# Kernel optimization log

Hardware: AMD Instinct MI355X
Metric: run time of the kernel (lower is better)

The kernel has to match this reference:

```python
import jax, jax.numpy as jnp
import numpy as np

DIM = 512
NUM_HEADS = 8
HEAD_DIM = DIM // NUM_HEADS
B, S = 2, 2048


def setup_inputs() -> dict:
    key = jax.random.key(0)
    ks = jax.random.split(key, 16)
    scale = 1.0 / np.sqrt(DIM)
    inp = {
        "x": jax.random.normal(ks[0], (B, S, DIM), dtype=jnp.float32),
        "Qexpl": jax.random.normal(ks[1], (B, S, DIM), dtype=jnp.float32),
        "Kexpl": jax.random.normal(ks[2], (B, S, DIM), dtype=jnp.float32),
        "fl": jax.random.uniform(ks[3], (B,), dtype=jnp.float32),
        "fu": jax.random.uniform(ks[4], (B,), dtype=jnp.float32),
        "age": jax.random.uniform(ks[5], (B,), dtype=jnp.float32),
        "gender": jax.random.uniform(ks[6], (B,), dtype=jnp.float32),
        # Linear params: weight stored as [out, in] like torch; y = x @ W.T + b
        "Wq": jax.random.normal(ks[7], (DIM, DIM), dtype=jnp.float32) * scale,
        "bq": jnp.zeros((DIM,), dtype=jnp.float32),
        "Wk": jax.random.normal(ks[8], (DIM, DIM), dtype=jnp.float32) * scale,
        "bk": jnp.zeros((DIM,), dtype=jnp.float32),
        "Wv": jax.random.normal(ks[9], (DIM, DIM), dtype=jnp.float32) * scale,
        "bv": jnp.zeros((DIM,), dtype=jnp.float32),
        "Wo": jax.random.normal(ks[10], (DIM, DIM), dtype=jnp.float32) * scale,
        "bo": jnp.zeros((DIM,), dtype=jnp.float32),
    }
    return inp


def reference(x, Qexpl, Kexpl, fl, fu, age, gender, Wq, bq, Wk, bk, Wv, bv, Wo, bo):
    # drofe_fn is None -> Q/K projections used directly.
    Q = Qexpl @ Wq.T + bq            # [B, S, D]
    K = Kexpl @ Wk.T + bk            # [B, S, D]
    V = x @ Wv.T + bv                # [B, S, D]

    def split_heads(t):  # [B, S, D] -> [B, H, S, hd]
        return t.reshape(B, S, NUM_HEADS, HEAD_DIM).transpose(0, 2, 1, 3)

    Qh, Kh, Vh = split_heads(Q), split_heads(K), split_heads(V)
    scale = 1.0 / np.sqrt(HEAD_DIM).astype(np.float32)
    scores = jnp.einsum("bhqd,bhkd->bhqk", Qh, Kh) * scale  # [B, H, S, S]
    weights = jax.nn.softmax(scores, axis=-1)
    attn = jnp.einsum("bhqk,bhkd->bhqd", weights, Vh)        # [B, H, S, hd]
    attn = attn.transpose(0, 2, 1, 3).reshape(B, S, DIM)
    return attn @ Wo.T + bo
```

## Files before the change

kernel.cpp:

```cpp
#include <hip/hip_runtime.h>
#include <hip/hip_bf16.h>

typedef unsigned short ushort_t;
typedef __attribute__((ext_vector_type(8))) short bf16x8;
typedef __attribute__((ext_vector_type(4))) float f32x4;

__device__ __forceinline__ ushort_t f2bf(float f) {
    union { float f; unsigned u; } v; v.f = f;
    unsigned r = v.u + 0x7FFF + ((v.u >> 16) & 1);
    return (ushort_t)(r >> 16);
}
__device__ __forceinline__ bf16x8 ld8(const ushort_t* p) { return *(const bf16x8*)p; }

__device__ __forceinline__ unsigned cvt2(float x, float y) {
    __hip_bfloat162 h = __float22bfloat162_rn(make_float2(x, y));
    unsigned r; __builtin_memcpy(&r, &h, 4); return r;
}
__device__ __forceinline__ bf16x8 pack8f(float4 a, float4 b) {
    union { unsigned u[4]; bf16x8 v; } o;
    o.u[0] = cvt2(a.x, a.y); o.u[1] = cvt2(a.z, a.w);
    o.u[2] = cvt2(b.x, b.y); o.u[3] = cvt2(b.z, b.w);
    return o.v;
}

__device__ __forceinline__ void gload_lds16(const ushort_t* g, ushort_t* l) {
    __builtin_amdgcn_global_load_lds(
        (const __attribute__((address_space(1))) void*)g,
        (__attribute__((address_space(3))) void*)l, 16, 0, 0);
}

__global__ __launch_bounds__(256, 2)
void proj_qkv_kernel(const float* __restrict__ Qe, const float* __restrict__ Ke,
                     const float* __restrict__ x,
                     const float* __restrict__ Wq, const float* __restrict__ Wk,
                     const float* __restrict__ Wv,
                     const float* __restrict__ bq, const float* __restrict__ bk,
                     const float* __restrict__ bv,
                     ushort_t* __restrict__ Qo, ushort_t* __restrict__ Ko,
                     ushort_t* __restrict__ Vt)
{
    __shared__ ushort_t smem[2 * 128 * 72];
    ushort_t* lA = smem;
    ushort_t* lB = smem + 128 * 72;

    const int z = blockIdx.z;
    const float* A = (z == 0) ? Qe : (z == 1) ? Ke : x;
    const float* W = (z == 0) ? Wq : (z == 1) ? Wk : Wv;
    const float* bias = (z == 0) ? bq : (z == 1) ? bk : bv;

    const int m0 = blockIdx.y * 128, n0 = blockIdx.x * 128;
    const int t = threadIdx.x;
    const int lane = t & 63, wave = t >> 6;
    const int wm = (wave & 1) * 64, wn = (wave >> 1) * 64;
    const int fr = lane & 15, quad = lane >> 4;

    f32x4 acc[4][4] = {};
    float4 fa[4][2], fw[4][2];

#pragma unroll
    for (int i = 0; i < 4; ++i) {
        int s = i * 256 + t;
        int r = s >> 3, jp = s & 7;
        const float* pa = A + (size_t)(m0 + r) * 512 + jp * 8;
        fa[i][0] = *(const float4*)pa; fa[i][1] = *(const float4*)(pa + 4);
        const float* pw = W + (size_t)(n0 + r) * 512 + jp * 8;
        fw[i][0] = *(const float4*)pw; fw[i][1] = *(const float4*)(pw + 4);
    }

    for (int kk = 0; kk < 8; ++kk) {
        if (kk) __syncthreads();
#pragma unroll
        for (int i = 0; i < 4; ++i) {
            int s = i * 256 + t;
            int r = s >> 3, jp = s & 7;
            *(bf16x8*)(lA + r * 72 + jp * 8) = pack8f(fa[i][0], fa[i][1]);
            *(bf16x8*)(lB + r * 72 + jp * 8) = pack8f(fw[i][0], fw[i][1]);
        }
        __syncthreads();
        if (kk < 7) {
            int k0 = (kk + 1) * 64;
#pragma unroll
            for (int i = 0; i < 4; ++i) {
                int s = i * 256 + t;
                int r = s >> 3, jp = s & 7;
                const float* pa = A + (size_t)(m0 + r) * 512 + k0 + jp * 8;
                fa[i][0] = *(const float4*)pa; fa[i][1] = *(const float4*)(pa + 4);
                const float* pw = W + (size_t)(n0 + r) * 512 + k0 + jp * 8;
                fw[i][0] = *(const float4*)pw; fw[i][1] = *(const float4*)(pw + 4);
            }
        }

#pragma unroll
        for (int ks = 0; ks < 2; ++ks) {
            bf16x8 af[4], bfrag[4];
#pragma unroll
            for (int mt = 0; mt < 4; ++mt)
                af[mt] = ld8(lA + (wm + mt * 16 + fr) * 72 + (ks * 4 + quad) * 8);
#pragma unroll
            for (int nt = 0; nt < 4; ++nt)
                bfrag[nt] = ld8(lB + (wn + nt * 16 + fr) * 72 + (ks * 4 + quad) * 8);
#pragma unroll
            for (int mt = 0; mt < 4; ++mt)
#pragma unroll
                for (int nt = 0; nt < 4; ++nt)
                    acc[mt][nt] = __builtin_amdgcn_mfma_f32_16x16x32_bf16(
                        af[mt], bfrag[nt], acc[mt][nt], 0, 0, 0);
        }
    }

    const float C1 = 0.125f * 1.44269504088896340736f;
    if (z != 2) {
        ushort_t* dst = (z == 0) ? Qo : Ko;
#pragma unroll
        for (int nt = 0; nt < 4; ++nt) {
            int n = n0 + wn + nt * 16 + fr;
            float bb = bias[n];
#pragma unroll
            for (int mt = 0; mt < 4; ++mt) {
                int mb = m0 + wm + mt * 16 + quad * 4;
                if (z == 0) {
#pragma unroll
                    for (int r = 0; r < 4; ++r)
                        dst[(size_t)(mb + r) * 512 + n] = f2bf((acc[mt][nt][r] + bb) * C1);
                } else {
#pragma unroll
                    for (int r = 0; r < 4; ++r)
                        dst[(size_t)(mb + r) * 512 + n] = f2bf(acc[mt][nt][r] + bb);
                }
            }
        }
    } else {
        __syncthreads();
        ushort_t* lT = smem;
#pragma unroll
        for (int nt = 0; nt < 4; ++nt) {
            int nl = wn + nt * 16 + fr;
            float bb = bias[n0 + nl];
#pragma unroll
            for (int mt = 0; mt < 4; ++mt) {
                int tm = wm + mt * 16 + quad * 4;
#pragma unroll
                for (int r = 0; r < 4; ++r) {
                    int tl = tm + r;
                    int sg = 8 * (tl & 15) + ((tl >> 4) & 7);
                    lT[nl * 136 + sg] = f2bf(acc[mt][nt][r] + bb);
                }
            }
        }
        __syncthreads();
        const int bidx = m0 >> 11, m0t = m0 & 2047;
#pragma unroll
        for (int i = 0; i < 8; ++i) {
            int s = i * 256 + t;
            int row = s >> 4, c = s & 15;
            int n = n0 + row;
            int h = n >> 6, d = n & 63;
            bf16x8 v = ld8(lT + row * 136 + c * 8);
            *(bf16x8*)(Vt + ((size_t)((bidx * 8 + h) * 64 + d)) * 2048 + m0t + c * 8) = v;
        }
    }
}

__global__ __launch_bounds__(256, 2)
void gemm_o_kernel(const ushort_t* __restrict__ A, const float* __restrict__ W,
                   const float* __restrict__ bias, float* __restrict__ dst)
{
    __shared__ ushort_t lA[64 * 72];
    __shared__ ushort_t lB[64 * 72];
    const int m0 = blockIdx.y * 64, n0 = blockIdx.x * 64;
    const int t = threadIdx.x;
    const int lane = t & 63, wave = t >> 6;
    const int wm = (wave & 1) * 32, wn = (wave >> 1) * 32;
    const int fr = lane & 15, quad = lane >> 4;

    f32x4 acc[2][2] = {};
    bf16x8 va[2];
    float4 fw[2][2];

#pragma unroll
    for (int i = 0; i < 2; ++i) {
        int s = i * 256 + t;
        int r = s >> 3, jp = s & 7;
        va[i] = ld8(A + (size_t)(m0 + r) * 512 + jp * 8);
        const float* p = W + (size_t)(n0 + r) * 512 + jp * 8;
        fw[i][0] = *(const float4*)p; fw[i][1] = *(const float4*)(p + 4);
    }

    for (int kk = 0; kk < 8; ++kk) {
        if (kk) __syncthreads();
#pragma unroll
        for (int i = 0; i < 2; ++i) {
            int s = i * 256 + t;
            int r = s >> 3, jp = s & 7;
            *(bf16x8*)(lA + r * 72 + jp * 8) = va[i];
            *(bf16x8*)(lB + r * 72 + jp * 8) = pack8f(fw[i][0], fw[i][1]);
        }
        __syncthreads();
        if (kk < 7) {
            int k0 = (kk + 1) * 64;
#pragma unroll
            for (int i = 0; i < 2; ++i) {
                int s = i * 256 + t;
                int r = s >> 3, jp = s & 7;
                va[i] = ld8(A + (size_t)(m0 + r) * 512 + k0 + jp * 8);
                const float* p = W + (size_t)(n0 + r) * 512 + k0 + jp * 8;
                fw[i][0] = *(const float4*)p; fw[i][1] = *(const float4*)(p + 4);
            }
        }

        bf16x8 af[2][2], bfrag[2][2];
#pragma unroll
        for (int ks = 0; ks < 2; ++ks) {
#pragma unroll
            for (int mt = 0; mt < 2; ++mt)
                af[mt][ks] = ld8(lA + (wm + mt * 16 + fr) * 72 + (ks * 4 + quad) * 8);
#pragma unroll
            for (int nt = 0; nt < 2; ++nt)
                bfrag[nt][ks] = ld8(lB + (wn + nt * 16 + fr) * 72 + (ks * 4 + quad) * 8);
        }
#pragma unroll
        for (int ks = 0; ks < 2; ++ks)
#pragma unroll
            for (int mt = 0; mt < 2; ++mt)
#pragma unroll
                for (int nt = 0; nt < 2; ++nt)
                    acc[mt][nt] = __builtin_amdgcn_mfma_f32_16x16x32_bf16(
                        af[mt][ks], bfrag[nt][ks], acc[mt][nt], 0, 0, 0);
    }

#pragma unroll
    for (int nt = 0; nt < 2; ++nt) {
        int n = n0 + wn + nt * 16 + fr;
        float bb = bias[n];
#pragma unroll
        for (int mt = 0; mt < 2; ++mt) {
            int mb = m0 + wm + mt * 16 + quad * 4;
#pragma unroll
            for (int r = 0; r < 4; ++r)
                dst[(size_t)(mb + r) * 512 + n] = acc[mt][nt][r] + bb;
        }
    }
}

__global__ __launch_bounds__(256, 3)
void attn_kernel(const ushort_t* __restrict__ Q, const ushort_t* __restrict__ K,
                 const ushort_t* __restrict__ Vt, float* __restrict__ Opart,
                 float* __restrict__ Lsum)
{
    __shared__ ushort_t lK[128 * 64];
    __shared__ ushort_t lV[64 * 128];
    __shared__ ushort_t lP[64 * 128];

    const int b = blockIdx.z >> 1, half = blockIdx.z & 1;
    const int h = blockIdx.y;
    const int q0 = blockIdx.x * 64;
    const int kvbase = half * 1024;
    const int t = threadIdx.x;
    const int lane = t & 63, w = t >> 6;
    const int wq = w * 16;
    const int fr = lane & 15, quad = lane >> 4;
    const int fr7 = fr & 7;

    bf16x8 aq[2];
    {
        const ushort_t* qp = Q + (size_t)(b * 2048 + q0 + wq + fr) * 512 + h * 64 + quad * 8;
        aq[0] = ld8(qp);
        aq[1] = ld8(qp + 32);
    }

    const int krl = w * 32 + (lane >> 3);
    const ushort_t* kg = K + (size_t)(b * 2048 + kvbase + krl) * 512 + h * 64
                           + (lane & 7) * 8;
    ushort_t* lk_wr = lK + krl * 64 + (((lane & 7) ^ (krl & 7)) << 3);

    const int vrl = w * 4 + (lane >> 4);
    const ushort_t* vbase = Vt + (size_t)((b * 8 + h) * 64 + vrl) * 2048 + kvbase
                              + (((lane & 15) ^ (vrl & 7)) << 3);

    const ushort_t* kr0 = lK + fr * 64 + ((quad ^ fr7) << 3);
    const ushort_t* kr1 = lK + fr * 64 + (((4 + quad) ^ fr7) << 3);
    const ushort_t* vr[4];
    const ushort_t* pr[4];
#pragma unroll
    for (int ks = 0; ks < 4; ++ks) {
        int cs = (((ks * 4 + quad) ^ fr7) << 3);
        vr[ks] = lV + fr * 128 + cs;
        pr[ks] = lP + (wq + fr) * 128 + cs;
    }
    ushort_t* pw[4];
#pragma unroll
    for (int r = 0; r < 4; ++r) {
        int row = wq + quad * 4 + r;
        pw[r] = lP + row * 128 + ((fr ^ (row & 7)) << 3);
    }

    bf16x8 kreg[4];
#pragma unroll
    for (int i = 0; i < 4; ++i)
        kreg[i] = ld8(kg + (size_t)(i * 8) * 512);
#pragma unroll
    for (int i = 0; i < 4; ++i)
        *(bf16x8*)(lk_wr + i * 8 * 64) = kreg[i];
    __syncthreads();

    f32x4 oacc[4] = {};
    float lpart[4] = {};

    for (int tt = 0; tt < 8; ++tt) {
        const int kv = tt << 7;

#pragma unroll
        for (int i = 0; i < 4; ++i)
            gload_lds16(vbase + kv + (size_t)(i * 16) * 2048, lV + (i * 16 + w * 4) * 128);
        __builtin_amdgcn_sched_barrier(0);
        if (tt < 7) {
#pragma unroll
            for (int i = 0; i < 4; ++i)
                kreg[i] = ld8(kg + (size_t)(kv + 128 + i * 8) * 512);
        }
        __builtin_amdgcn_sched_barrier(0);

        f32x4 sc[8] = {};
#pragma unroll
        for (int nt = 0; nt < 8; ++nt) {
            bf16x8 kb = ld8(kr0 + nt * 16 * 64);
            sc[nt] = __builtin_amdgcn_mfma_f32_16x16x32_bf16(aq[0], kb, sc[nt], 0, 0, 0);
        }
#pragma unroll
        for (int nt = 0; nt < 8; ++nt) {
            bf16x8 kb = ld8(kr1 + nt * 16 * 64);
            sc[nt] = __builtin_amdgcn_mfma_f32_16x16x32_bf16(aq[1], kb, sc[nt], 0, 0, 0);
        }

#pragma unroll
        for (int r = 0; r < 4; ++r) {
            float pv[8]; float acc = 0.f;
#pragma unroll
            for (int nt = 0; nt < 8; ++nt) { pv[nt] = exp2f(sc[nt][r]); acc += pv[nt]; }
            lpart[r] += acc;
            union { unsigned u[4]; bf16x8 v; } pu;
            pu.u[0] = cvt2(pv[0], pv[1]); pu.u[1] = cvt2(pv[2], pv[3]);
            pu.u[2] = cvt2(pv[4], pv[5]); pu.u[3] = cvt2(pv[6], pv[7]);
            *(bf16x8*)pw[r] = pu.v;
        }

        if (tt < 7) asm volatile("s_waitcnt vmcnt(4)" ::: "memory");
        else        asm volatile("s_waitcnt vmcnt(0)" ::: "memory");
        __builtin_amdgcn_s_barrier();
        __builtin_amdgcn_sched_barrier(0);

        if (tt < 7) {
#pragma unroll
            for (int i = 0; i < 4; ++i)
                *(bf16x8*)(lk_wr + i * 8 * 64) = kreg[i];
        }

#pragma unroll
        for (int ks = 0; ks < 4; ++ks) {
            bf16x8 ap = ld8(pr[ks]);
#pragma unroll
            for (int nt = 0; nt < 4; ++nt) {
                bf16x8 vb = ld8(vr[ks] + nt * 16 * 128);
                oacc[nt] = __builtin_amdgcn_mfma_f32_16x16x32_bf16(ap, vb, oacc[nt], 0, 0, 0);
            }
        }
        __syncthreads();
    }

#pragma unroll
    for (int r = 0; r < 4; ++r) {
        float rs = lpart[r];
#pragma unroll
        for (int o = 1; o < 16; o <<= 1)
            rs += __shfl_xor(rs, o, 64);
        int qrow = q0 + wq + quad * 4 + r;
        float* od = Opart + ((size_t)(half * 2 + b) * 2048 + qrow) * 512 + h * 64;
#pragma unroll
        for (int nt = 0; nt < 4; ++nt)
            od[nt * 16 + fr] = oacc[nt][r];
        if (fr == 0)
            Lsum[((half * 2 + b) * 8 + h) * 2048 + qrow] = rs;
    }
}

__global__ __launch_bounds__(256)
void merge_kernel(const float* __restrict__ Opart, const float* __restrict__ Lsum,
                  ushort_t* __restrict__ Ows)
{
    int gid = blockIdx.x * 256 + threadIdx.x;
    int row = gid >> 7;
    int c4 = (gid & 127) << 2;
    int b = row >> 11, q = row & 2047;
    int h = c4 >> 6;
    float l0 = Lsum[(b * 8 + h) * 2048 + q];
    float l1 = Lsum[((2 + b) * 8 + h) * 2048 + q];
    float inv = 1.f / (l0 + l1);
    float4 o0 = *(const float4*)(Opart + (size_t)row * 512 + c4);
    float4 o1 = *(const float4*)(Opart + (size_t)(row + 4096) * 512 + c4);
    union { unsigned u[2]; } o;
    o.u[0] = cvt2((o0.x + o1.x) * inv, (o0.y + o1.y) * inv);
    o.u[1] = cvt2((o0.z + o1.z) * inv, (o0.w + o1.w) * inv);
    unsigned* dst = (unsigned*)(Ows + (size_t)row * 512 + c4);
    dst[0] = o.u[0];
    dst[1] = o.u[1];
}

extern "C" void kernel_launch(void* const* d_in, const int* in_sizes, int n_in,
                              void* d_out, int out_size, void* d_ws, size_t ws_size,
                              hipStream_t stream) {
    const float* x   = (const float*)d_in[0];
    const float* Qe  = (const float*)d_in[1];
    const float* Ke  = (const float*)d_in[2];
    const float* Wq  = (const float*)d_in[7];
    const float* bq  = (const float*)d_in[8];
    const float* Wk  = (const float*)d_in[9];
    const float* bk  = (const float*)d_in[10];
    const float* Wv  = (const float*)d_in[11];
    const float* bv  = (const float*)d_in[12];
    const float* Wo  = (const float*)d_in[13];
    const float* bo  = (const float*)d_in[14];

    const size_t NTOK = 2 * 2048;
    const size_t ACT = NTOK * 512;

    ushort_t* p = (ushort_t*)d_ws;
    ushort_t* Qws = p; p += ACT;
    ushort_t* Kws = p; p += ACT;
    ushort_t* Vt  = p; p += ACT;
    ushort_t* Ows = p; p += ACT;
    float* Opart = (float*)p;
    float* Lsum  = Opart + 2 * ACT;

    proj_qkv_kernel<<<dim3(4, 32, 3), 256, 0, stream>>>(Qe, Ke, x, Wq, Wk, Wv,
                                                        bq, bk, bv, Qws, Kws, Vt);
    attn_kernel<<<dim3(32, 8, 4), 256, 0, stream>>>(Qws, Kws, Vt, Opart, Lsum);
    merge_kernel<<<dim3(2048), 256, 0, stream>>>(Opart, Lsum, Ows);
    gemm_o_kernel<<<dim3(8, 64), 256, 0, stream>>>(Ows, Wo, bo, (float*)d_out);
}
```

Measured before the change: 168.4 us.

## Keep softmax probabilities in registers and fuse merge into output projection

The attention kernel now computes S^T by swapping the MFMA operands, so each lane's score accumulators line up with the A-operand layout of the PV MFMA. The exponentiated probabilities are packed to bf16 in registers instead of going through an LDS P tile, and the V staging permutation in the QKV projection is changed to match. The LDS saving allows raising occupancy to 4 blocks per CU, and setprio is added around the MFMA sections. The separate merge kernel is removed: the output GEMM now reads both fp32 partial outputs and row sums directly, normalizing and converting to bf16 while staging. That reads twice as many fp32 bytes per GEMM tile in exchange for dropping one launch and a round trip through memory.

```diff
diff --git a/kernel.cpp b/kernel.cpp
--- a/kernel.cpp
+++ b/kernel.cpp
@@ -142,7 +142,7 @@
 #pragma unroll
                 for (int r = 0; r < 4; ++r) {
                     int tl = tm + r;
-                    int sg = 8 * (tl & 15) + ((tl >> 4) & 7);
+                    int sg = (tl & 96) + ((tl & 12) << 1) + ((tl >> 4 & 1) << 2) + (tl & 3);
                     lT[nl * 136 + sg] = f2bf(acc[mt][nt][r] + bb);
                 }
             }
@@ -162,8 +162,9 @@
 }
 
 __global__ __launch_bounds__(256, 2)
-void gemm_o_kernel(const ushort_t* __restrict__ A, const float* __restrict__ W,
-                   const float* __restrict__ bias, float* __restrict__ dst)
+void gemm_o_kernel(const float* __restrict__ Opart, const float* __restrict__ Lsum,
+                   const float* __restrict__ W, const float* __restrict__ bias,
+                   float* __restrict__ dst)
 {
     __shared__ ushort_t lA[64 * 72];
     __shared__ ushort_t lB[64 * 72];
@@ -172,16 +173,23 @@
     const int lane = t & 63, wave = t >> 6;
     const int wm = (wave & 1) * 32, wn = (wave >> 1) * 32;
     const int fr = lane & 15, quad = lane >> 4;
+    const int bq_ = m0 >> 11;
+    const int qq0 = m0 & 2047;
 
     f32x4 acc[2][2] = {};
-    bf16x8 va[2];
-    float4 fw[2][2];
+    float4 fo0[2][2], fo1[2][2], fw[2][2];
+    float l0[2], l1[2];
 
 #pragma unroll
     for (int i = 0; i < 2; ++i) {
         int s = i * 256 + t;
         int r = s >> 3, jp = s & 7;
-        va[i] = ld8(A + (size_t)(m0 + r) * 512 + jp * 8);
+        const float* p0 = Opart + (size_t)(m0 + r) * 512 + jp * 8;
+        fo0[i][0] = *(const float4*)p0;        fo0[i][1] = *(const float4*)(p0 + 4);
+        fo1[i][0] = *(const float4*)(p0 + 4096 * 512);
+        fo1[i][1] = *(const float4*)(p0 + 4096 * 512 + 4);
+        l0[i] = Lsum[(bq_ * 8 + 0) * 2048 + qq0 + r];
+        l1[i] = Lsum[((2 + bq_) * 8 + 0) * 2048 + qq0 + r];
         const float* p = W + (size_t)(n0 + r) * 512 + jp * 8;
         fw[i][0] = *(const float4*)p; fw[i][1] = *(const float4*)(p + 4);
     }
@@ -192,7 +200,16 @@
         for (int i = 0; i < 2; ++i) {
             int s = i * 256 + t;
             int r = s >> 3, jp = s & 7;
-            *(bf16x8*)(lA + r * 72 + jp * 8) = va[i];
+            float inv = 1.f / (l0[i] + l1[i]);
+            float4 a0 = make_float4((fo0[i][0].x + fo1[i][0].x) * inv,
+                                    (fo0[i][0].y + fo1[i][0].y) * inv,
+                                    (fo0[i][0].z + fo1[i][0].z) * inv,
+                                    (fo0[i][0].w + fo1[i][0].w) * inv);
+            float4 a1 = make_float4((fo0[i][1].x + fo1[i][1].x) * inv,
+                                    (fo0[i][1].y + fo1[i][1].y) * inv,
+                                    (fo0[i][1].z + fo1[i][1].z) * inv,
+                                    (fo0[i][1].w + fo1[i][1].w) * inv);
+            *(bf16x8*)(lA + r * 72 + jp * 8) = pack8f(a0, a1);
             *(bf16x8*)(lB + r * 72 + jp * 8) = pack8f(fw[i][0], fw[i][1]);
         }
         __syncthreads();
@@ -202,7 +219,12 @@
             for (int i = 0; i < 2; ++i) {
                 int s = i * 256 + t;
                 int r = s >> 3, jp = s & 7;
-                va[i] = ld8(A + (size_t)(m0 + r) * 512 + k0 + jp * 8);
+                const float* p0 = Opart + (size_t)(m0 + r) * 512 + k0 + jp * 8;
+                fo0[i][0] = *(const float4*)p0;        fo0[i][1] = *(const float4*)(p0 + 4);
+                fo1[i][0] = *(const float4*)(p0 + 4096 * 512);
+                fo1[i][1] = *(const float4*)(p0 + 4096 * 512 + 4);
+                l0[i] = Lsum[(bq_ * 8 + kk + 1) * 2048 + qq0 + r];
+                l1[i] = Lsum[((2 + bq_) * 8 + kk + 1) * 2048 + qq0 + r];
                 const float* p = W + (size_t)(n0 + r) * 512 + k0 + jp * 8;
                 fw[i][0] = *(const float4*)p; fw[i][1] = *(const float4*)(p + 4);
             }
@@ -242,14 +264,13 @@
     }
 }
 
-__global__ __launch_bounds__(256, 3)
+__global__ __launch_bounds__(256, 4)
 void attn_kernel(const ushort_t* __restrict__ Q, const ushort_t* __restrict__ K,
                  const ushort_t* __restrict__ Vt, float* __restrict__ Opart,
                  float* __restrict__ Lsum)
 {
     __shared__ ushort_t lK[128 * 64];
     __shared__ ushort_t lV[64 * 128];
-    __shared__ ushort_t lP[64 * 128];
 
     const int b = blockIdx.z >> 1, half = blockIdx.z & 1;
     const int h = blockIdx.y;
@@ -279,20 +300,11 @@
 
     const ushort_t* kr0 = lK + fr * 64 + ((quad ^ fr7) << 3);
     const ushort_t* kr1 = lK + fr * 64 + (((4 + quad) ^ fr7) << 3);
-    const ushort_t* vr[4];
-    const ushort_t* pr[4];
-#pragma unroll
-    for (int ks = 0; ks < 4; ++ks) {
-        int cs = (((ks * 4 + quad) ^ fr7) << 3);
-        vr[ks] = lV + fr * 128 + cs;
-        pr[ks] = lP + (wq + fr) * 128 + cs;
-    }
-    ushort_t* pw[4];
-#pragma unroll
-    for (int r = 0; r < 4; ++r) {
-        int row = wq + quad * 4 + r;
-        pw[r] = lP + row * 128 + ((fr ^ (row & 7)) << 3);
-    }
+    const ushort_t* vr0 = lV + fr * 128 + (((0 * 4 + quad) ^ fr7) << 3);
+    const ushort_t* vr1 = lV + fr * 128 + (((1 * 4 + quad) ^ fr7) << 3);
+    const ushort_t* vr2 = lV + fr * 128 + (((2 * 4 + quad) ^ fr7) << 3);
+    const ushort_t* vr3 = lV + fr * 128 + (((3 * 4 + quad) ^ fr7) << 3);
+    const ushort_t* vr[4] = { vr0, vr1, vr2, vr3 };
 
     bf16x8 kreg[4];
 #pragma unroll
@@ -304,7 +316,7 @@
     __syncthreads();
 
     f32x4 oacc[4] = {};
-    float lpart[4] = {};
+    float lsum = 0.f;
 
     for (int tt = 0; tt < 8; ++tt) {
         const int kv = tt << 7;
@@ -321,88 +333,65 @@
         __builtin_amdgcn_sched_barrier(0);
 
         f32x4 sc[8] = {};
+        __builtin_amdgcn_s_setprio(1);
 #pragma unroll
         for (int nt = 0; nt < 8; ++nt) {
             bf16x8 kb = ld8(kr0 + nt * 16 * 64);
-            sc[nt] = __builtin_amdgcn_mfma_f32_16x16x32_bf16(aq[0], kb, sc[nt], 0, 0, 0);
+            sc[nt] = __builtin_amdgcn_mfma_f32_16x16x32_bf16(kb, aq[0], sc[nt], 0, 0, 0);
         }
 #pragma unroll
         for (int nt = 0; nt < 8; ++nt) {
             bf16x8 kb = ld8(kr1 + nt * 16 * 64);
-            sc[nt] = __builtin_amdgcn_mfma_f32_16x16x32_bf16(aq[1], kb, sc[nt], 0, 0, 0);
-        }
-
-#pragma unroll
-        for (int r = 0; r < 4; ++r) {
-            float pv[8]; float acc = 0.f;
-#pragma unroll
-            for (int nt = 0; nt < 8; ++nt) { pv[nt] = exp2f(sc[nt][r]); acc += pv[nt]; }
-            lpart[r] += acc;
-            union { unsigned u[4]; bf16x8 v; } pu;
-            pu.u[0] = cvt2(pv[0], pv[1]); pu.u[1] = cvt2(pv[2], pv[3]);
-            pu.u[2] = cvt2(pv[4], pv[5]); pu.u[3] = cvt2(pv[6], pv[7]);
-            *(bf16x8*)pw[r] = pu.v;
-        }
+            sc[nt] = __builtin_amdgcn_mfma_f32_16x16x32_bf16(kb, aq[1], sc[nt], 0, 0, 0);
+        }
+        __builtin_amdgcn_s_setprio(0);
 
         if (tt < 7) asm volatile("s_waitcnt vmcnt(4)" ::: "memory");
         else        asm volatile("s_waitcnt vmcnt(0)" ::: "memory");
         __builtin_amdgcn_s_barrier();
         __builtin_amdgcn_sched_barrier(0);
 
-        if (tt < 7) {
-#pragma unroll
-            for (int i = 0; i < 4; ++i)
-                *(bf16x8*)(lk_wr + i * 8 * 64) = kreg[i];
-        }
-
+        __builtin_amdgcn_s_setprio(1);
 #pragma unroll
         for (int ks = 0; ks < 4; ++ks) {
-            bf16x8 ap = ld8(pr[ks]);
+            float p0[4], p1[4];
+#pragma unroll
+            for (int r = 0; r < 4; ++r) p0[r] = exp2f(sc[2 * ks][r]);
+#pragma unroll
+            for (int r = 0; r < 4; ++r) p1[r] = exp2f(sc[2 * ks + 1][r]);
+            lsum += ((p0[0] + p0[1]) + (p0[2] + p0[3]))
+                  + ((p1[0] + p1[1]) + (p1[2] + p1[3]));
+            union { unsigned u[4]; bf16x8 v; } pa;
+            pa.u[0] = cvt2(p0[0], p0[1]); pa.u[1] = cvt2(p0[2], p0[3]);
+            pa.u[2] = cvt2(p1[0], p1[1]); pa.u[3] = cvt2(p1[2], p1[3]);
 #pragma unroll
             for (int nt = 0; nt < 4; ++nt) {
                 bf16x8 vb = ld8(vr[ks] + nt * 16 * 128);
-                oacc[nt] = __builtin_amdgcn_mfma_f32_16x16x32_bf16(ap, vb, oacc[nt], 0, 0, 0);
-            }
-        }
+                oacc[nt] = __builtin_amdgcn_mfma_f32_16x16x32_bf16(pa.v, vb, oacc[nt], 0, 0, 0);
+            }
+            if (ks == 0 && tt < 7) {
+#pragma unroll
+                for (int i = 0; i < 4; ++i)
+                    *(bf16x8*)(lk_wr + i * 8 * 64) = kreg[i];
+            }
+        }
+        __builtin_amdgcn_s_setprio(0);
         __syncthreads();
     }
 
+    float rs = lsum;
+    rs += __shfl_xor(rs, 16, 64);
+    rs += __shfl_xor(rs, 32, 64);
 #pragma unroll
     for (int r = 0; r < 4; ++r) {
-        float rs = lpart[r];
-#pragma unroll
-        for (int o = 1; o < 16; o <<= 1)
-            rs += __shfl_xor(rs, o, 64);
         int qrow = q0 + wq + quad * 4 + r;
         float* od = Opart + ((size_t)(half * 2 + b) * 2048 + qrow) * 512 + h * 64;
 #pragma unroll
         for (int nt = 0; nt < 4; ++nt)
             od[nt * 16 + fr] = oacc[nt][r];
-        if (fr == 0)
-            Lsum[((half * 2 + b) * 8 + h) * 2048 + qrow] = rs;
-    }
-}
-
-__global__ __launch_bounds__(256)
-void merge_kernel(const float* __restrict__ Opart, const float* __restrict__ Lsum,
-                  ushort_t* __restrict__ Ows)
-{
-    int gid = blockIdx.x * 256 + threadIdx.x;
-    int row = gid >> 7;
-    int c4 = (gid & 127) << 2;
-    int b = row >> 11, q = row & 2047;
-    int h = c4 >> 6;
-    float l0 = Lsum[(b * 8 + h) * 2048 + q];
-    float l1 = Lsum[((2 + b) * 8 + h) * 2048 + q];
-    float inv = 1.f / (l0 + l1);
-    float4 o0 = *(const float4*)(Opart + (size_t)row * 512 + c4);
-    float4 o1 = *(const float4*)(Opart + (size_t)(row + 4096) * 512 + c4);
-    union { unsigned u[2]; } o;
-    o.u[0] = cvt2((o0.x + o1.x) * inv, (o0.y + o1.y) * inv);
-    o.u[1] = cvt2((o0.z + o1.z) * inv, (o0.w + o1.w) * inv);
-    unsigned* dst = (unsigned*)(Ows + (size_t)row * 512 + c4);
-    dst[0] = o.u[0];
-    dst[1] = o.u[1];
+    }
+    if (lane < 16)
+        Lsum[((half * 2 + b) * 8 + h) * 2048 + q0 + wq + lane] = rs;
 }
 
 extern "C" void kernel_launch(void* const* d_in, const int* in_sizes, int n_in,
@@ -427,13 +416,11 @@
     ushort_t* Qws = p; p += ACT;
     ushort_t* Kws = p; p += ACT;
     ushort_t* Vt  = p; p += ACT;
-    ushort_t* Ows = p; p += ACT;
     float* Opart = (float*)p;
     float* Lsum  = Opart + 2 * ACT;
 
     proj_qkv_kernel<<<dim3(4, 32, 3), 256, 0, stream>>>(Qe, Ke, x, Wq, Wk, Wv,
                                                         bq, bk, bv, Qws, Kws, Vt);
     attn_kernel<<<dim3(32, 8, 4), 256, 0, stream>>>(Qws, Kws, Vt, Opart, Lsum);
-    merge_kernel<<<dim3(2048), 256, 0, stream>>>(Opart, Lsum, Ows);
-    gemm_o_kernel<<<dim3(8, 64), 256, 0, stream>>>(Ows, Wo, bo, (float*)d_out);
-}
+    gemm_o_kernel<<<dim3(8, 64), 256, 0, stream>>>(Opart, Lsum, Wo, bo, (float*)d_out);
+}
```

Measured after the change: 168.2 us. Within noise of the previous version (-0.1%).
